# Kernel optimization log

Hardware: AMD Instinct MI355X
Metric: run time of the kernel (lower is better)

Reference implementation:

```python
import jax, jax.numpy as jnp
import numpy as np

D_MODEL = 1024
D_KV = 64
N_HEADS = 16
KV_HEADS = 4
G = N_HEADS // KV_HEADS
NUM_BUCKETS = 32
MAX_DISTANCE = 128


def _relative_position_bucket(relative_position, bidirectional=True,
                              num_buckets=NUM_BUCKETS, max_distance=MAX_DISTANCE):
    # Faithful port of T5Attention._relative_position_bucket
    relative_buckets = jnp.zeros_like(relative_position)
    if bidirectional:
        num_buckets //= 2
        relative_buckets = (relative_position > 0).astype(jnp.int32) * num_buckets
        relative_position = jnp.abs(relative_position)
    else:
        relative_position = -jnp.minimum(relative_position, 0)
    max_exact = num_buckets // 2
    is_small = relative_position < max_exact
    rel_if_large = max_exact + (
        jnp.log(relative_position.astype(jnp.float32) / max_exact)
        / np.log(max_distance / max_exact) * (num_buckets - max_exact)
    ).astype(jnp.int32)
    rel_if_large = jnp.minimum(rel_if_large, num_buckets - 1)
    return relative_buckets + jnp.where(is_small, relative_position, rel_if_large)


def setup_inputs() -> dict:
    key = jax.random.key(0)
    ks = jax.random.split(key, 6)
    B, S = 2, 2048
    inner = N_HEADS * D_KV
    sc = 1.0 / np.sqrt(D_MODEL)
    return {
        "hidden_states": jax.random.normal(ks[0], (B, S, D_MODEL), dtype=jnp.float32),
        "Wq": jax.random.normal(ks[1], (D_MODEL, inner), dtype=jnp.float32) * sc,
        "Wk": jax.random.normal(ks[2], (D_MODEL, inner), dtype=jnp.float32) * sc,
        "Wv": jax.random.normal(ks[3], (D_MODEL, inner), dtype=jnp.float32) * sc,
        "Wo": jax.random.normal(ks[4], (inner, D_MODEL), dtype=jnp.float32) * sc,
        "rel_bias": jax.random.normal(ks[5], (NUM_BUCKETS, N_HEADS), dtype=jnp.float32) * 0.1,
    }


def reference(hidden_states, Wq, Wk, Wv, Wo, rel_bias):
    B, S, _ = hidden_states.shape

    def split_heads(x):  # [B,S,inner] -> [B,H,S,Dk]
        return x.reshape(B, S, N_HEADS, D_KV).transpose(0, 2, 1, 3)

    q = split_heads(hidden_states @ Wq)
    k = split_heads(hidden_states @ Wk)
    v = split_heads(hidden_states @ Wv)

    # head index = g * KV_HEADS + h (einops 'b (g h) ...' with h=kv_heads)
    gq = q.reshape(B, G, KV_HEADS, S, D_KV)
    gk = k.reshape(B, G, KV_HEADS, S, D_KV).mean(axis=1)  # [B,Hkv,S,Dk]
    # einsum sums over g (as in torch.einsum 'bghnd,bhsd->bhns'); no 1/sqrt(d) in T5
    scores = jnp.einsum('bghnd,bhsd->bhns', gq, gk)  # [B,Hkv,S,S]

    # T5 relative position bias (bidirectional, encoder)
    ctx = jnp.arange(S)[:, None]
    mem = jnp.arange(S)[None, :]
    buckets = _relative_position_bucket(mem - ctx, bidirectional=True)
    bias = rel_bias[buckets]                # [S,S,H]
    bias = bias.transpose(2, 0, 1)[None]    # [1,H,S,S]
    gbias = bias.reshape(1, G, KV_HEADS, S, S).mean(axis=1)  # [1,Hkv,S,S]

    scores = scores + gbias
    attn = jax.nn.softmax(scores.astype(jnp.float32), axis=-1).astype(scores.dtype)

    # repeat grouped attn weights back to full heads: 'b h n s -> b (g h) n s'
    attn_full = jnp.tile(attn, (1, G, 1, 1))  # [B,H,S,S]
    ctx_out = jnp.einsum('bhns,bhsd->bhnd', attn_full, v)  # [B,H,S,Dk]
    ctx_out = ctx_out.transpose(0, 2, 1, 3).reshape(B, S, N_HEADS * D_KV)
    return ctx_out @ Wo  # [B,S,D_MODEL]
```

## Files before the change

kernel.cpp:

```cpp
#include <hip/hip_runtime.h>
#include <math.h>


typedef __bf16 bf16_t;
typedef bf16_t bf16x8 __attribute__((ext_vector_type(8)));
typedef bf16_t bf16x4 __attribute__((ext_vector_type(4)));
typedef float f32x4 __attribute__((ext_vector_type(4)));

#define MFMA16(a, b, c) __builtin_amdgcn_mfma_f32_16x16x32_bf16(a, b, c, 0, 0, 0)

typedef __attribute__((address_space(1))) void gvoid;
typedef __attribute__((address_space(3))) void svoid;
__device__ __forceinline__ void gld16(const void* g, void* l) {
    __builtin_amdgcn_global_load_lds((gvoid*)g, (svoid*)l, 16, 0, 0);
}

__global__ __launch_bounds__(256) void prep_all(const float* __restrict__ hs,
                                                const float* __restrict__ Wq,
                                                const float* __restrict__ Wk,
                                                const float* __restrict__ Wv,
                                                const float* __restrict__ Wo,
                                                const float* __restrict__ rel_bias,
                                                bf16_t* __restrict__ hs_hi,
                                                bf16_t* __restrict__ hs_lo,
                                                bf16_t* __restrict__ Thi,
                                                bf16_t* __restrict__ Tlo,
                                                bf16_t* __restrict__ WvT,
                                                bf16_t* __restrict__ WoT,
                                                float* __restrict__ btab) {
    __shared__ float sm[2048];
    const int r = blockIdx.x, t = threadIdx.x;
    if (r < 4096) {
        size_t idx = ((size_t)r * 256 + t) * 4;
        float4 v = *(const float4*)(hs + idx);
        bf16x4 h, l;
        h[0] = (bf16_t)v.x; l[0] = (bf16_t)(v.x - (float)h[0]);
        h[1] = (bf16_t)v.y; l[1] = (bf16_t)(v.y - (float)h[1]);
        h[2] = (bf16_t)v.z; l[2] = (bf16_t)(v.z - (float)h[2]);
        h[3] = (bf16_t)v.w; l[3] = (bf16_t)(v.w - (float)h[3]);
        *(bf16x4*)(hs_hi + idx) = h;
        *(bf16x4*)(hs_lo + idx) = l;
    } else if (r < 4224) {
        const int k0 = (r - 4096) * 8;
        const int h = t >> 6, j2 = t & 63;
        bf16x8 qh8, ql8, kh8, kl8;
#pragma unroll
        for (int kk = 0; kk < 8; ++kk) {
            const float* wqr = Wq + (size_t)(k0 + kk) * 1024;
            const float* wkr = Wk + (size_t)(k0 + kk) * 1024;
            float sq = 0.f, sk = 0.f;
#pragma unroll
            for (int g = 0; g < 4; ++g) {
                int c = (g * 4 + h) * 64 + j2;
                sq += wqr[c];
                sk += wkr[c];
            }
            sk *= 0.25f;
            bf16_t qh = (bf16_t)sq;
            qh8[kk] = qh;
            ql8[kk] = (bf16_t)(sq - (float)qh);
            bf16_t kh = (bf16_t)sk;
            kh8[kk] = kh;
            kl8[kk] = (bf16_t)(sk - (float)kh);
        }
        *(bf16x8*)(Thi + (size_t)t * 1024 + k0) = qh8;
        *(bf16x8*)(Tlo + (size_t)t * 1024 + k0) = ql8;
        *(bf16x8*)(Thi + (size_t)(256 + t) * 1024 + k0) = kh8;
        *(bf16x8*)(Tlo + (size_t)(256 + t) * 1024 + k0) = kl8;
    } else if (r < 6272) {
        int rr = r - 4224;
        const float* src = (rr < 1024) ? Wv : Wo;
        bf16_t* dst = (rr < 1024) ? WvT : WoT;
        if (rr >= 1024) rr -= 1024;
        int bx = (rr & 31) * 32, by = (rr >> 5) * 32;
        int tx = t & 31, ty = t >> 5;
        float(*tile)[33] = (float(*)[33])sm;
#pragma unroll
        for (int i = 0; i < 32; i += 8)
            tile[ty + i][tx] = src[(size_t)(by + ty + i) * 1024 + bx + tx];
        __syncthreads();
#pragma unroll
        for (int i = 0; i < 32; i += 8)
            dst[(size_t)(bx + ty + i) * 1024 + by + tx] = (bf16_t)tile[tx][ty + i];
    } else {
        int idx = (r - 6272) * 256 + t;
        if (idx >= 4095) return;
        int delta = idx - 2047;
        int bucket = (delta > 0) ? 16 : 0;
        int arp = delta < 0 ? -delta : delta;
        int rb;
        if (arp < 8) {
            rb = arp;
        } else {
            float tt = (logf((float)arp * 0.125f) / 2.772588722239781f) * 8.0f;
            int ri = 8 + (int)tt;
            rb = ri < 15 ? ri : 15;
        }
        bucket += rb;
#pragma unroll
        for (int h = 0; h < 4; ++h) {
            float s = 0.25f * (rel_bias[bucket * 16 + h] + rel_bias[bucket * 16 + h + 4] +
                               rel_bias[bucket * 16 + h + 8] + rel_bias[bucket * 16 + h + 12]);
            btab[h * 4608 + idx] = s;
        }
    }
}

__global__ __launch_bounds__(256, 1) void proj_qkv(const bf16_t* __restrict__ Ah,
                                                   const bf16_t* __restrict__ Al,
                                                   const bf16_t* __restrict__ Bh,
                                                   const bf16_t* __restrict__ Bl,
                                                   const bf16_t* __restrict__ WvT,
                                                   bf16_t* __restrict__ Qhi,
                                                   bf16_t* __restrict__ Qlo,
                                                   bf16_t* __restrict__ Kbh,
                                                   bf16_t* __restrict__ Kbl,
                                                   bf16_t* __restrict__ Vb) {
    __shared__ bf16_t pool[36864];
    const int K = 1024, nk = 32;
    const int t = threadIdx.x;
    const int w = t >> 6, lane = t & 63;
    const int lr = lane & 15, q = lane >> 4;
    const int l = blockIdx.y * 16 + blockIdx.x;
    const int nl = (l & 7) * 64 + (l >> 3);
    const int bx = nl & 15;
    const int m0 = (nl >> 4) * 128;
    const bool qk = bx < 8;
    const int n0 = qk ? bx * 64 : (bx - 8) * 128;
    const int mw = (w & 1) * 64;
    f32x4 acc[4][4] = {};

    const int rA = t & 127, cA0 = t >> 7, cA1 = 2 + (t >> 7);
    const size_t oA0 = (size_t)(m0 + rA) * K + cA0 * 8;
    const size_t oA1 = (size_t)(m0 + rA) * K + cA1 * 8;
    const int rBq = t & 63, cBq = t >> 6;
    const size_t oBq = (size_t)(n0 + rBq) * K + cBq * 8;
    const size_t oBv0 = (size_t)(n0 + rA) * K + cA0 * 8;
    const size_t oBv1 = (size_t)(n0 + rA) * K + cA1 * 8;

    auto stage = [&](int bf, int kidx) {
        bf16_t* base = &pool[bf * 12288];
        const int k0 = kidx * 32;
        gld16(Ah + oA0 + k0, base + t * 8);
        gld16(Ah + oA1 + k0, base + (256 + t) * 8);
        if (qk) {
            gld16(Al + oA0 + k0, base + 4096 + t * 8);
            gld16(Al + oA1 + k0, base + 4096 + (256 + t) * 8);
            gld16(Bh + oBq + k0, base + 8192 + t * 8);
            gld16(Bl + oBq + k0, base + 10240 + t * 8);
        } else {
            gld16(WvT + oBv0 + k0, base + 4096 + t * 8);
            gld16(WvT + oBv1 + k0, base + 4096 + (256 + t) * 8);
        }
    };

    stage(0, 0);
    stage(1, 1);
    stage(2, 2);
    if (qk)
        asm volatile("s_waitcnt vmcnt(12)" ::: "memory");
    else
        asm volatile("s_waitcnt vmcnt(8)" ::: "memory");
    __builtin_amdgcn_s_barrier();

    int cur = 0;
    for (int it = 0; it < nk; ++it) {
        const bf16_t* base = &pool[cur * 12288];
        if (qk) {
            const int nw = (w >> 1) * 32;
            bf16x8 ah[4], al[4], bh[2], bl[2];
#pragma unroll
            for (int i = 0; i < 4; ++i) {
                int sa = (q * 128 + mw + i * 16 + lr) * 8;
                ah[i] = *(const bf16x8*)&base[sa];
                al[i] = *(const bf16x8*)&base[4096 + sa];
            }
#pragma unroll
            for (int j = 0; j < 2; ++j) {
                int sb = (q * 64 + nw + j * 16 + lr) * 8;
                bh[j] = *(const bf16x8*)&base[8192 + sb];
                bl[j] = *(const bf16x8*)&base[10240 + sb];
            }
            asm volatile("s_waitcnt lgkmcnt(0)" ::: "memory");
            if (it < nk - 2)
                asm volatile("s_waitcnt vmcnt(6)" ::: "memory");
            else
                asm volatile("s_waitcnt vmcnt(0)" ::: "memory");
            __builtin_amdgcn_s_barrier();
            if (it + 3 < nk) stage(cur, it + 3);
#pragma unroll
            for (int i = 0; i < 4; ++i)
#pragma unroll
                for (int j = 0; j < 2; ++j) {
                    acc[i][j] = MFMA16(ah[i], bh[j], acc[i][j]);
                    acc[i][j] = MFMA16(ah[i], bl[j], acc[i][j]);
                    acc[i][j] = MFMA16(al[i], bh[j], acc[i][j]);
                }
        } else {
            const int nw = (w >> 1) * 64;
            bf16x8 af[4], bfv[4];
#pragma unroll
            for (int i = 0; i < 4; ++i)
                af[i] = *(const bf16x8*)&base[(q * 128 + mw + i * 16 + lr) * 8];
#pragma unroll
            for (int j = 0; j < 4; ++j)
                bfv[j] = *(const bf16x8*)&base[4096 + (q * 128 + nw + j * 16 + lr) * 8];
            asm volatile("s_waitcnt lgkmcnt(0)" ::: "memory");
            if (it < nk - 2)
                asm volatile("s_waitcnt vmcnt(4)" ::: "memory");
            else
                asm volatile("s_waitcnt vmcnt(0)" ::: "memory");
            __builtin_amdgcn_s_barrier();
            if (it + 3 < nk) stage(cur, it + 3);
#pragma unroll
            for (int i = 0; i < 4; ++i)
#pragma unroll
                for (int j = 0; j < 4; ++j) acc[i][j] = MFMA16(af[i], bfv[j], acc[i][j]);
        }
        cur = (cur == 2) ? 0 : cur + 1;
    }

    if (qk) {
        const int nwq = (w >> 1) * 32;
#pragma unroll
        for (int i = 0; i < 4; ++i) {
            int row = m0 + mw + i * 16 + q * 4;
#pragma unroll
            for (int j = 0; j < 2; ++j) {
                int col = n0 + nwq + j * 16 + lr;
#pragma unroll
                for (int reg = 0; reg < 4; ++reg) {
                    float x = acc[i][j][reg];
                    int token = row + reg;
                    bf16_t hi = (bf16_t)x;
                    bf16_t lo = (bf16_t)(x - (float)hi);
                    if (col < 256) {
                        size_t o = (size_t)token * 256 + col;
                        Qhi[o] = hi;
                        Qlo[o] = lo;
                    } else {
                        int hc = col - 256;
                        int hh = hc >> 6, d = hc & 63;
                        int b = token >> 11, s = token & 2047;
                        int it2 = s >> 6, sl = s & 63;
                        size_t o = ((size_t)((b * 4 + hh) * 32 + it2)) * 4096 +
                                   (size_t)((d >> 3) * 64 + sl) * 8 + (d & 7);
                        Kbh[o] = hi;
                        Kbl[o] = lo;
                    }
                }
            }
        }
    } else {
        const int nwq = (w >> 1) * 64;
#pragma unroll
        for (int i = 0; i < 4; ++i) {
            int row = m0 + mw + i * 16 + q * 4;
            int b = row >> 11, s = row & 2047;
            int it2 = s >> 6, sc2 = (s >> 3) & 7, si = s & 7;
#pragma unroll
            for (int j = 0; j < 4; ++j) {
                int col = n0 + nwq + j * 16 + lr;
                int hh = (col >> 6) & 3, g = col >> 8, d = col & 63;
                size_t o = ((size_t)((b * 4 + hh) * 32 + it2)) * 16384 +
                           (size_t)(sc2 * 256 + g * 64 + d) * 8 + si;
                bf16x4 pv;
#pragma unroll
                for (int reg = 0; reg < 4; ++reg) pv[reg] = (bf16_t)acc[i][j][reg];
                *(bf16x4*)(Vb + o) = pv;
            }
        }
    }
}

__global__ __launch_bounds__(256, 1) void gemm_out(const bf16_t* __restrict__ A,
                                                   const bf16_t* __restrict__ BT,
                                                   float* __restrict__ C,
                                                   int M, int N, int K) {
    __shared__ bf16_t pool[36864];
    const int t = threadIdx.x;
    const int w = t >> 6, lane = t & 63;
    const int lr = lane & 15, q = lane >> 4;
    const int l = blockIdx.y * 16 + blockIdx.x;
    const int nl = (l & 7) * 64 + (l >> 3);
    const int m0 = (nl >> 4) * 128, n0 = (nl & 15) * 64;
    const int mw = (w & 1) * 64, nw = (w >> 1) * 32;
    f32x4 acc[4][2] = {};
    const int nk = K >> 6;

    const int rA = t & 127, cA = t >> 7;
    const int rB = t & 63, cB = t >> 6;
    const bf16_t* gA = A + (size_t)(m0 + rA) * K + cA * 8;
    const bf16_t* gB = BT + (size_t)(n0 + rB) * K + cB * 8;

    auto stage = [&](int bf, int kidx) {
        bf16_t* base = &pool[bf * 12288];
        const int k0 = kidx * 64;
#pragma unroll
        for (int j = 0; j < 4; ++j)
            gld16(gA + k0 + j * 16, base + ((cA + 2 * j) * 128 + rA) * 8);
        gld16(gB + k0, base + 8192 + (cB * 64 + rB) * 8);
        gld16(gB + k0 + 32, base + 8192 + ((cB + 4) * 64 + rB) * 8);
    };

    stage(0, 0);
    stage(1, 1);
    stage(2, 2);
    asm volatile("s_waitcnt vmcnt(12)" ::: "memory");
    __builtin_amdgcn_s_barrier();

    int cur = 0;
    for (int it = 0; it < nk; ++it) {
        const bf16_t* base = &pool[cur * 12288];
        bf16x8 af[4][2], bfv[2][2];
#pragma unroll
        for (int i = 0; i < 4; ++i)
#pragma unroll
            for (int kb = 0; kb < 2; ++kb)
                af[i][kb] = *(const bf16x8*)&base[((kb * 4 + q) * 128 + mw + i * 16 + lr) * 8];
#pragma unroll
        for (int j = 0; j < 2; ++j)
#pragma unroll
            for (int kb = 0; kb < 2; ++kb)
                bfv[j][kb] =
                    *(const bf16x8*)&base[8192 + ((kb * 4 + q) * 64 + nw + j * 16 + lr) * 8];
        asm volatile("s_waitcnt lgkmcnt(0)" ::: "memory");
        if (it < nk - 2)
            asm volatile("s_waitcnt vmcnt(6)" ::: "memory");
        else
            asm volatile("s_waitcnt vmcnt(0)" ::: "memory");
        __builtin_amdgcn_s_barrier();
        if (it + 3 < nk) stage(cur, it + 3);
#pragma unroll
        for (int i = 0; i < 4; ++i)
#pragma unroll
            for (int j = 0; j < 2; ++j)
#pragma unroll
                for (int kb = 0; kb < 2; ++kb)
                    acc[i][j] = MFMA16(af[i][kb], bfv[j][kb], acc[i][j]);
        cur = (cur == 2) ? 0 : cur + 1;
    }

#pragma unroll
    for (int i = 0; i < 4; ++i) {
        int row = m0 + mw + i * 16 + q * 4;
#pragma unroll
        for (int j = 0; j < 2; ++j) {
            int col = n0 + nw + j * 16 + lr;
#pragma unroll
            for (int reg = 0; reg < 4; ++reg)
                C[(size_t)(row + reg) * N + col] = acc[i][j][reg];
        }
    }
}

__global__ __launch_bounds__(512, 1) void attn_mfma(const bf16_t* __restrict__ Qhi,
                                                    const bf16_t* __restrict__ Qlo,
                                                    const bf16_t* __restrict__ Kbh,
                                                    const bf16_t* __restrict__ Kbl,
                                                    const bf16_t* __restrict__ Vb,
                                                    const float* __restrict__ btab,
                                                    bf16_t* __restrict__ part0,
                                                    bf16_t* __restrict__ part1,
                                                    float* __restrict__ Sml) {
    __shared__ bf16_t Kh[2][4096], Kl[2][4096], Vsm[2][16384], Ps[8192];
    const int t = threadIdx.x, w = t >> 6, lane = t & 63;
    const int lr = lane & 15, q = lane >> 4;
    const int bl0 = blockIdx.x;
    const int blk = (bl0 & 7) * 32 + (bl0 >> 3);
    const int half = blk & 1, qt = (blk >> 1) & 15, h = (blk >> 5) & 3, b = blk >> 7;
    const int n0 = qt * 128;
    const int rowbase = n0 + w * 16;
    const int swz = (lr & 7) << 3;
    const int psb = w * 1024 + lr * 64;

    const size_t qrow = (size_t)(b * 2048 + rowbase + lr) * 256 + h * 64;
    bf16x8 aqh[2], aql[2];
#pragma unroll
    for (int kb = 0; kb < 2; ++kb) {
        aqh[kb] = *(const bf16x8*)(Qhi + qrow + kb * 32 + q * 8);
        aql[kb] = *(const bf16x8*)(Qlo + qrow + kb * 32 + q * 8);
    }

    const int tilebase = (b * 4 + h) * 32 + half * 16;
    const bf16_t* gK = Kbh + (size_t)tilebase * 4096;
    const bf16_t* gL = Kbl + (size_t)tilebase * 4096;
    const bf16_t* gV = Vb + (size_t)tilebase * 16384;
    const float* btabh = btab + h * 4608 + 2047;
    const float bpos = btabh[1024];
    const float bneg = btabh[-1024];

    auto stage = [&](int bf, int it) {
        gld16(gK + (size_t)it * 4096 + t * 8, &Kh[bf][t * 8]);
        gld16(gL + (size_t)it * 4096 + t * 8, &Kl[bf][t * 8]);
        const bf16_t* v0 = gV + (size_t)it * 16384;
#pragma unroll
        for (int j = 0; j < 4; ++j)
            gld16(v0 + (j * 512 + t) * 8, &Vsm[bf][(j * 512 + t) * 8]);
    };

    float m_r = -INFINITY, l_r = 0.f;
    f32x4 O[16] = {};

    stage(0, 0);
    __syncthreads();
    for (int it = 0; it < 16; ++it) {
        const int cur = it & 1;
        if (it + 1 < 16) stage(cur ^ 1, it + 1);
        const int s0g = half * 1024 + it * 64;

        f32x4 sc[4];
#pragma unroll
        for (int ct = 0; ct < 4; ++ct) {
            f32x4 z = {0.f, 0.f, 0.f, 0.f};
#pragma unroll
            for (int kb = 0; kb < 2; ++kb) {
                int sb = ((kb * 4 + q) * 64 + ct * 16 + lr) * 8;
                bf16x8 bh = *(const bf16x8*)&Kh[cur][sb];
                bf16x8 bl = *(const bf16x8*)&Kl[cur][sb];
                z = MFMA16(bh, aqh[kb], z);
                z = MFMA16(bh, aql[kb], z);
                z = MFMA16(bl, aqh[kb], z);
            }
            sc[ct] = z;
        }
        if (s0g - rowbase >= 143) {
#pragma unroll
            for (int ct = 0; ct < 4; ++ct)
#pragma unroll
                for (int reg = 0; reg < 4; ++reg) sc[ct][reg] += bpos;
        } else if (rowbase - s0g >= 154) {
#pragma unroll
            for (int ct = 0; ct < 4; ++ct)
#pragma unroll
                for (int reg = 0; reg < 4; ++reg) sc[ct][reg] += bneg;
        } else {
            const int dbase = (s0g + q * 4) - (rowbase + lr);
#pragma unroll
            for (int ct = 0; ct < 4; ++ct)
#pragma unroll
                for (int reg = 0; reg < 4; ++reg)
                    sc[ct][reg] += btabh[dbase + ct * 16 + reg];
        }

        float mt = fmaxf(fmaxf(sc[0][0], sc[0][1]), fmaxf(sc[0][2], sc[0][3]));
#pragma unroll
        for (int ct = 1; ct < 4; ++ct)
            mt = fmaxf(mt, fmaxf(fmaxf(sc[ct][0], sc[ct][1]), fmaxf(sc[ct][2], sc[ct][3])));
        mt = fmaxf(mt, __shfl_xor(mt, 16, 64));
        mt = fmaxf(mt, __shfl_xor(mt, 32, 64));

        float mn = fmaxf(m_r, mt);
        const bool noresc = (bool)__all(mn == m_r);
        float al = noresc ? 1.f : __expf(m_r - mn);
        m_r = mn;
        float rs = 0.f;
#pragma unroll
        for (int ct = 0; ct < 4; ++ct) {
            bf16x4 tq;
#pragma unroll
            for (int reg = 0; reg < 4; ++reg) {
                float p = __expf(sc[ct][reg] - mn);
                rs += p;
                tq[reg] = (bf16_t)p;
            }
            *(bf16x4*)&Ps[psb + ((ct * 16 + q * 4) ^ swz)] = tq;
        }
        rs += __shfl_xor(rs, 16, 64);
        rs += __shfl_xor(rs, 32, 64);
        l_r = l_r * al + rs;

        if (!noresc) {
#pragma unroll
            for (int nt = 0; nt < 16; ++nt)
#pragma unroll
                for (int reg = 0; reg < 4; ++reg) O[nt][reg] *= al;
        }

        bf16x8 pf0 = *(const bf16x8*)&Ps[psb + ((q * 8) ^ swz)];
        bf16x8 pf1 = *(const bf16x8*)&Ps[psb + ((32 + q * 8) ^ swz)];

#pragma unroll
        for (int nt = 0; nt < 16; ++nt) {
            f32x4 o = O[nt];
            bf16x8 v0 = *(const bf16x8*)&Vsm[cur][(q * 256 + nt * 16 + lr) * 8];
            o = MFMA16(v0, pf0, o);
            bf16x8 v1 = *(const bf16x8*)&Vsm[cur][((4 + q) * 256 + nt * 16 + lr) * 8];
            o = MFMA16(v1, pf1, o);
            O[nt] = o;
        }
        __syncthreads();
    }

    bf16_t* P = half ? part1 : part0;
    const float inv = 1.f / l_r;
    const int tokb = b * 2048 + rowbase;
#pragma unroll
    for (int G = 0; G < 4; ++G) {
#pragma unroll
        for (int g4 = 0; g4 < 4; ++g4) {
            int nt = G * 4 + g4;
            bf16x4 tq;
#pragma unroll
            for (int reg = 0; reg < 4; ++reg) tq[reg] = (bf16_t)(O[nt][reg] * inv);
            *(bf16x4*)&Ps[psb + ((g4 * 16 + q * 4) ^ swz)] = tq;
        }
#pragma unroll
        for (int i = 0; i < 2; ++i) {
            int row = i * 8 + (lane >> 3), cv = (lane & 7) * 8;
            bf16x8 fr = *(const bf16x8*)&Ps[w * 1024 + row * 64 + (cv ^ ((row & 7) << 3))];
            *(bf16x8*)(P + (size_t)(tokb + row) * 1024 + (G * 4 + h) * 64 + cv) = fr;
        }
    }
    if (lane < 16)
        Sml[half * 16384 + (size_t)(tokb + lane) * 4 + h] = m_r + logf(l_r);
}

__global__ __launch_bounds__(256) void combine_halves(bf16_t* __restrict__ p0,
                                                      const bf16_t* __restrict__ p1,
                                                      const float* __restrict__ Sml) {
    size_t flat = ((size_t)blockIdx.x * 256 + threadIdx.x) * 8;
    int tok = (int)(flat >> 10), c = (int)(flat & 1023), h = (c >> 6) & 3;
    float s0 = Sml[tok * 4 + h], s1 = Sml[16384 + tok * 4 + h];
    float M = fmaxf(s0, s1);
    float e0 = __expf(s0 - M), e1 = __expf(s1 - M);
    float r = 1.f / (e0 + e1);
    float w0 = e0 * r, w1 = e1 * r;
    bf16x8 a = *(bf16x8*)(p0 + flat);
    bf16x8 bb = *(const bf16x8*)(p1 + flat);
    bf16x8 o;
#pragma unroll
    for (int i = 0; i < 8; ++i) o[i] = (bf16_t)(w0 * (float)a[i] + w1 * (float)bb[i]);
    *(bf16x8*)(p0 + flat) = o;
}

extern "C" void kernel_launch(void* const* d_in, const int* in_sizes, int n_in,
                              void* d_out, int out_size, void* d_ws, size_t ws_size,
                              hipStream_t stream) {
    const float* hs = (const float*)d_in[0];
    const float* Wq = (const float*)d_in[1];
    const float* Wk = (const float*)d_in[2];
    const float* Wv = (const float*)d_in[3];
    const float* Wo = (const float*)d_in[4];
    const float* rb = (const float*)d_in[5];
    float* out = (float*)d_out;

    const size_t MB = 1 << 20;
    const size_t KB = 1 << 10;
    char* ws = (char*)d_ws;
    bf16_t* hs_hi = (bf16_t*)(ws);
    bf16_t* hs_lo = (bf16_t*)(ws + 8 * MB);
    bf16_t* WqkThi = (bf16_t*)(ws + 16 * MB);
    bf16_t* WqkTlo = (bf16_t*)(ws + 17 * MB);
    bf16_t* WvT = (bf16_t*)(ws + 18 * MB);
    bf16_t* WoT = (bf16_t*)(ws + 20 * MB);
    float* btab = (float*)(ws + 22 * MB);
    float* Sml = (float*)(ws + 22 * MB + 128 * KB);
    bf16_t* Qhi = (bf16_t*)(ws + 22 * MB + 256 * KB);
    bf16_t* Qlo = Qhi + (size_t)4096 * 256;
    bf16_t* Kbh = Qlo + (size_t)4096 * 256;
    bf16_t* Kbl = Kbh + (size_t)4096 * 256;
    bf16_t* Vb = Kbl + (size_t)4096 * 256;
    bf16_t* part0 = hs_hi;
    bf16_t* part1 = hs_lo;

    prep_all<<<6288, 256, 0, stream>>>(hs, Wq, Wk, Wv, Wo, rb, hs_hi, hs_lo, WqkThi,
                                       WqkTlo, WvT, WoT, btab);
    proj_qkv<<<dim3(16, 32), 256, 0, stream>>>(hs_hi, hs_lo, WqkThi, WqkTlo, WvT, Qhi,
                                               Qlo, Kbh, Kbl, Vb);
    attn_mfma<<<256, 512, 0, stream>>>(Qhi, Qlo, Kbh, Kbl, Vb, btab, part0, part1, Sml);
    combine_halves<<<2048, 256, 0, stream>>>(part0, part1, Sml);
    gemm_out<<<dim3(16, 32), 256, 0, stream>>>(part0, WoT, out, 4096, 1024, 1024);
}
```

Baseline: 217.5 us.

## Double proj_qkv threads and K-step, halving per-wave M tile

The QKV projection kernel now launches 512 threads per block instead of 256 and uses 8 waves. Each wave covers 32 rows instead of 64. The K step per pipeline stage doubles from 32 to 64, so there are 16 iterations instead of 32, and the LDS buffers double to 144 KB. The aim is more waves in flight for latency hiding and half as many barriers per tile. In exchange, per-wave register reuse drops and LDS usage grows, which limits residency to one block per CU.

```diff
diff --git a/kernel.cpp b/kernel.cpp
--- a/kernel.cpp
+++ b/kernel.cpp
@@ -106,7 +106,7 @@
     }
 }
 
-__global__ __launch_bounds__(256, 1) void proj_qkv(const bf16_t* __restrict__ Ah,
+__global__ __launch_bounds__(512, 1) void proj_qkv(const bf16_t* __restrict__ Ah,
                                                    const bf16_t* __restrict__ Al,
                                                    const bf16_t* __restrict__ Bh,
                                                    const bf16_t* __restrict__ Bl,
@@ -116,8 +116,8 @@
                                                    bf16_t* __restrict__ Kbh,
                                                    bf16_t* __restrict__ Kbl,
                                                    bf16_t* __restrict__ Vb) {
-    __shared__ bf16_t pool[36864];
-    const int K = 1024, nk = 32;
+    __shared__ bf16_t pool[73728];
+    const int K = 1024, nk = 16;
     const int t = threadIdx.x;
     const int w = t >> 6, lane = t & 63;
     const int lr = lane & 15, q = lane >> 4;
@@ -127,30 +127,30 @@
     const int m0 = (nl >> 4) * 128;
     const bool qk = bx < 8;
     const int n0 = qk ? bx * 64 : (bx - 8) * 128;
-    const int mw = (w & 1) * 64;
-    f32x4 acc[4][4] = {};
-
-    const int rA = t & 127, cA0 = t >> 7, cA1 = 2 + (t >> 7);
+    const int mw = (w & 3) * 32;
+    f32x4 acc[2][4] = {};
+
+    const int rA = t & 127, cA0 = t >> 7;
     const size_t oA0 = (size_t)(m0 + rA) * K + cA0 * 8;
-    const size_t oA1 = (size_t)(m0 + rA) * K + cA1 * 8;
-    const int rBq = t & 63, cBq = t >> 6;
-    const size_t oBq = (size_t)(n0 + rBq) * K + cBq * 8;
+    const size_t oA1 = (size_t)(m0 + rA) * K + (cA0 + 4) * 8;
+    const int rB = t & 63, cB = t >> 6;
+    const size_t oBq = (size_t)(n0 + rB) * K + cB * 8;
     const size_t oBv0 = (size_t)(n0 + rA) * K + cA0 * 8;
-    const size_t oBv1 = (size_t)(n0 + rA) * K + cA1 * 8;
+    const size_t oBv1 = (size_t)(n0 + rA) * K + (cA0 + 4) * 8;
 
     auto stage = [&](int bf, int kidx) {
-        bf16_t* base = &pool[bf * 12288];
-        const int k0 = kidx * 32;
-        gld16(Ah + oA0 + k0, base + t * 8);
-        gld16(Ah + oA1 + k0, base + (256 + t) * 8);
+        bf16_t* base = &pool[bf * 24576];
+        const int k0 = kidx * 64;
+        gld16(Ah + oA0 + k0, base + (cA0 * 128 + rA) * 8);
+        gld16(Ah + oA1 + k0, base + ((cA0 + 4) * 128 + rA) * 8);
         if (qk) {
-            gld16(Al + oA0 + k0, base + 4096 + t * 8);
-            gld16(Al + oA1 + k0, base + 4096 + (256 + t) * 8);
-            gld16(Bh + oBq + k0, base + 8192 + t * 8);
-            gld16(Bl + oBq + k0, base + 10240 + t * 8);
+            gld16(Al + oA0 + k0, base + 8192 + (cA0 * 128 + rA) * 8);
+            gld16(Al + oA1 + k0, base + 8192 + ((cA0 + 4) * 128 + rA) * 8);
+            gld16(Bh + oBq + k0, base + 16384 + (cB * 64 + rB) * 8);
+            gld16(Bl + oBq + k0, base + 20480 + (cB * 64 + rB) * 8);
         } else {
-            gld16(WvT + oBv0 + k0, base + 4096 + t * 8);
-            gld16(WvT + oBv1 + k0, base + 4096 + (256 + t) * 8);
+            gld16(WvT + oBv0 + k0, base + 8192 + (cA0 * 128 + rA) * 8);
+            gld16(WvT + oBv1 + k0, base + 8192 + ((cA0 + 4) * 128 + rA) * 8);
         }
     };
 
@@ -165,22 +165,26 @@
 
     int cur = 0;
     for (int it = 0; it < nk; ++it) {
-        const bf16_t* base = &pool[cur * 12288];
+        const bf16_t* base = &pool[cur * 24576];
         if (qk) {
-            const int nw = (w >> 1) * 32;
-            bf16x8 ah[4], al[4], bh[2], bl[2];
-#pragma unroll
-            for (int i = 0; i < 4; ++i) {
-                int sa = (q * 128 + mw + i * 16 + lr) * 8;
-                ah[i] = *(const bf16x8*)&base[sa];
-                al[i] = *(const bf16x8*)&base[4096 + sa];
-            }
-#pragma unroll
-            for (int j = 0; j < 2; ++j) {
-                int sb = (q * 64 + nw + j * 16 + lr) * 8;
-                bh[j] = *(const bf16x8*)&base[8192 + sb];
-                bl[j] = *(const bf16x8*)&base[10240 + sb];
-            }
+            const int nw = (w >> 2) * 32;
+            bf16x8 ah[2][2], al[2][2], bh[2][2], bl[2][2];
+#pragma unroll
+            for (int i = 0; i < 2; ++i)
+#pragma unroll
+                for (int kb = 0; kb < 2; ++kb) {
+                    int sa = ((kb * 4 + q) * 128 + mw + i * 16 + lr) * 8;
+                    ah[i][kb] = *(const bf16x8*)&base[sa];
+                    al[i][kb] = *(const bf16x8*)&base[8192 + sa];
+                }
+#pragma unroll
+            for (int j = 0; j < 2; ++j)
+#pragma unroll
+                for (int kb = 0; kb < 2; ++kb) {
+                    int sb = ((kb * 4 + q) * 64 + nw + j * 16 + lr) * 8;
+                    bh[j][kb] = *(const bf16x8*)&base[16384 + sb];
+                    bl[j][kb] = *(const bf16x8*)&base[20480 + sb];
+                }
             asm volatile("s_waitcnt lgkmcnt(0)" ::: "memory");
             if (it < nk - 2)
                 asm volatile("s_waitcnt vmcnt(6)" ::: "memory");
@@ -189,22 +193,30 @@
             __builtin_amdgcn_s_barrier();
             if (it + 3 < nk) stage(cur, it + 3);
 #pragma unroll
-            for (int i = 0; i < 4; ++i)
-#pragma unroll
-                for (int j = 0; j < 2; ++j) {
-                    acc[i][j] = MFMA16(ah[i], bh[j], acc[i][j]);
-                    acc[i][j] = MFMA16(ah[i], bl[j], acc[i][j]);
-                    acc[i][j] = MFMA16(al[i], bh[j], acc[i][j]);
-                }
+            for (int i = 0; i < 2; ++i)
+#pragma unroll
+                for (int j = 0; j < 2; ++j)
+#pragma unroll
+                    for (int kb = 0; kb < 2; ++kb) {
+                        acc[i][j] = MFMA16(ah[i][kb], bh[j][kb], acc[i][j]);
+                        acc[i][j] = MFMA16(ah[i][kb], bl[j][kb], acc[i][j]);
+                        acc[i][j] = MFMA16(al[i][kb], bh[j][kb], acc[i][j]);
+                    }
         } else {
-            const int nw = (w >> 1) * 64;
-            bf16x8 af[4], bfv[4];
-#pragma unroll
-            for (int i = 0; i < 4; ++i)
-                af[i] = *(const bf16x8*)&base[(q * 128 + mw + i * 16 + lr) * 8];
+            const int nw = (w >> 2) * 64;
+            bf16x8 af[2][2], bfv[4][2];
+#pragma unroll
+            for (int i = 0; i < 2; ++i)
+#pragma unroll
+                for (int kb = 0; kb < 2; ++kb)
+                    af[i][kb] =
+                        *(const bf16x8*)&base[((kb * 4 + q) * 128 + mw + i * 16 + lr) * 8];
 #pragma unroll
             for (int j = 0; j < 4; ++j)
-                bfv[j] = *(const bf16x8*)&base[4096 + (q * 128 + nw + j * 16 + lr) * 8];
+#pragma unroll
+                for (int kb = 0; kb < 2; ++kb)
+                    bfv[j][kb] = *(const bf16x8*)&base[8192 + ((kb * 4 + q) * 128 + nw +
+                                                              j * 16 + lr) * 8];
             asm volatile("s_waitcnt lgkmcnt(0)" ::: "memory");
             if (it < nk - 2)
                 asm volatile("s_waitcnt vmcnt(4)" ::: "memory");
@@ -213,17 +225,20 @@
             __builtin_amdgcn_s_barrier();
             if (it + 3 < nk) stage(cur, it + 3);
 #pragma unroll
-            for (int i = 0; i < 4; ++i)
-#pragma unroll
-                for (int j = 0; j < 4; ++j) acc[i][j] = MFMA16(af[i], bfv[j], acc[i][j]);
+            for (int i = 0; i < 2; ++i)
+#pragma unroll
+                for (int j = 0; j < 4; ++j)
+#pragma unroll
+                    for (int kb = 0; kb < 2; ++kb)
+                        acc[i][j] = MFMA16(af[i][kb], bfv[j][kb], acc[i][j]);
         }
         cur = (cur == 2) ? 0 : cur + 1;
     }
 
     if (qk) {
-        const int nwq = (w >> 1) * 32;
-#pragma unroll
-        for (int i = 0; i < 4; ++i) {
+        const int nwq = (w >> 2) * 32;
+#pragma unroll
+        for (int i = 0; i < 2; ++i) {
             int row = m0 + mw + i * 16 + q * 4;
 #pragma unroll
             for (int j = 0; j < 2; ++j) {
@@ -252,15 +267,15 @@
             }
         }
     } else {
-        const int nwq = (w >> 1) * 64;
-#pragma unroll
-        for (int i = 0; i < 4; ++i) {
+        const int nwv = (w >> 2) * 64;
+#pragma unroll
+        for (int i = 0; i < 2; ++i) {
             int row = m0 + mw + i * 16 + q * 4;
             int b = row >> 11, s = row & 2047;
             int it2 = s >> 6, sc2 = (s >> 3) & 7, si = s & 7;
 #pragma unroll
             for (int j = 0; j < 4; ++j) {
-                int col = n0 + nwq + j * 16 + lr;
+                int col = n0 + nwv + j * 16 + lr;
                 int hh = (col >> 6) & 3, g = col >> 8, d = col & 63;
                 size_t o = ((size_t)((b * 4 + hh) * 32 + it2)) * 16384 +
                            (size_t)(sc2 * 256 + g * 64 + d) * 8 + si;
@@ -566,7 +581,7 @@
 
     prep_all<<<6288, 256, 0, stream>>>(hs, Wq, Wk, Wv, Wo, rb, hs_hi, hs_lo, WqkThi,
                                        WqkTlo, WvT, WoT, btab);
-    proj_qkv<<<dim3(16, 32), 256, 0, stream>>>(hs_hi, hs_lo, WqkThi, WqkTlo, WvT, Qhi,
+    proj_qkv<<<dim3(16, 32), 512, 0, stream>>>(hs_hi, hs_lo, WqkThi, WqkTlo, WvT, Qhi,
                                                Qlo, Kbh, Kbl, Vb);
     attn_mfma<<<256, 512, 0, stream>>>(Qhi, Qlo, Kbh, Kbl, Vb, btab, part0, part1, Sml);
     combine_halves<<<2048, 256, 0, stream>>>(part0, part1, Sml);
```

New measurement: 217.0 us. No clear change (-0.2%).
